# Kernel optimization log

Measured on AMD Instinct MI355X. Metric: run time of the kernel, lower is better.

## Reference

```python
import jax, jax.numpy as jnp
import numpy as np

EPS = 1e-08

def setup_inputs() -> dict:
    key = jax.random.key(0)
    ks = jax.random.split(key, 5)
    B, T, D, L = 8, 4096, 1024, 24
    data = jax.random.normal(ks[0], (B, T, D), dtype=jnp.float32)
    W_enc = jax.random.normal(ks[1], (L, D), dtype=jnp.float32) * (1.0 / np.sqrt(D))
    b_enc = jax.random.normal(ks[2], (L,), dtype=jnp.float32) * 0.01
    W_dec = jax.random.normal(ks[3], (D, L), dtype=jnp.float32) * (1.0 / np.sqrt(L))
    b_dec = jax.random.normal(ks[4], (D,), dtype=jnp.float32) * 0.01
    ecs = jnp.array([0.1], dtype=jnp.float32)  # error_correction_strength
    ep = jnp.array([1.0], dtype=jnp.float32)   # energy_preservation
    return {"data": data, "W_enc": W_enc, "b_enc": b_enc,
            "W_dec": W_dec, "b_dec": b_dec,
            "error_correction_strength": ecs, "energy_preservation": ep}

def _l2(x):
    return jnp.linalg.norm(x, axis=-1, keepdims=True)

def reference(data, W_enc, b_enc, W_dec, b_dec, error_correction_strength, energy_preservation):
    ecs = error_correction_strength[0]
    ep = energy_preservation[0]
    # --- encode_to_lattice ---
    in_e = _l2(data)                                   # [B,T,1]
    proj = jnp.einsum('btd,ld->btl', data, W_enc) + b_enc
    lattice_points = jnp.round(proj / ecs) * ecs       # quantize to lattice grid
    out_e = _l2(lattice_points)
    lattice = lattice_points * (in_e / (out_e + EPS)) * ep
    # --- decode_from_lattice ---
    in_e2 = _l2(lattice)
    corrected = jnp.where(jnp.abs(lattice) > ecs, lattice, 0.0)
    res = jnp.einsum('btl,dl->btd', corrected, W_dec) + b_dec
    out_e2 = _l2(res)
    return res * (in_e2 / (out_e2 + EPS)) * ep
```

## Files before the change

### kernel.cpp

```cpp
#include <hip/hip_runtime.h>
#include <math.h>

#define EPS 1e-8f


__global__ void prep_transpose(const float* __restrict__ W_enc, float* __restrict__ wt) {
    int i = blockIdx.x * 256 + threadIdx.x;
    if (i < 24576) {
        int k = i / 24, l = i - k * 24;
        wt[i] = W_enc[l * 1024 + k];
    }
}

__global__ void prep_gram(const float* __restrict__ Wd, const float* __restrict__ bd,
                          float* __restrict__ G, float* __restrict__ h, float* __restrict__ bb) {
    int b = blockIdx.x;
    int lane = threadIdx.x;
    float s = 0.f;
    if (b < 576) {
        int l = b / 24, m = b - (b / 24) * 24;
        for (int d = lane; d < 1024; d += 64) s = fmaf(Wd[d * 24 + l], Wd[d * 24 + m], s);
    } else if (b < 600) {
        int l = b - 576;
        for (int d = lane; d < 1024; d += 64) s = fmaf(Wd[d * 24 + l], bd[d], s);
    } else {
        for (int d = lane; d < 1024; d += 64) s = fmaf(bd[d], bd[d], s);
    }
    for (int off = 32; off; off >>= 1) s += __shfl_down(s, off);
    if (lane == 0) {
        if (b < 576) G[b] = s;
        else if (b < 600) h[b - 576] = s;
        else *bb = s;
    }
}


constexpr int LD_TILE   = 33;
constexpr int TILE_F    = 64 * LD_TILE;
constexpr int COMB_BASE = 4 * TILE_F;
constexpr int COMB_LD   = 65;
constexpr int SMEM_F    = COMB_BASE + 4 * 25 * COMB_LD;

__global__ __launch_bounds__(256, 2)
void leech_main(const float* __restrict__ data,
                const float* __restrict__ b_enc,
                const float* __restrict__ Wd,
                const float* __restrict__ b_dec,
                const float* __restrict__ ecs_p,
                const float* __restrict__ ep_p,
                const float* __restrict__ wt,
                const float* __restrict__ G,
                const float* __restrict__ h,
                const float* __restrict__ bbp,
                float* __restrict__ out)
{
    __shared__ float smem[SMEM_F];
    const int tid = threadIdx.x;
    const int w = tid >> 6;
    const int r = tid & 63;
    const int rowbase = blockIdx.x * 64;

    float* tile = smem + w * TILE_F;

    float proj[24];
#pragma unroll
    for (int l = 0; l < 24; ++l) proj[l] = 0.f;
    float ssq = 0.f;

    const int lrow = r >> 3;
    const int lk   = (r & 7) * 4;

    for (int sc = 0; sc < 8; ++sc) {
        const int k0 = w * 256 + sc * 32;
#pragma unroll
        for (int it = 0; it < 8; ++it) {
            const int row = it * 8 + lrow;
            const float4 v = *reinterpret_cast<const float4*>(
                data + (size_t)(rowbase + row) * 1024 + k0 + lk);
            float* t = tile + row * LD_TILE + lk;
            t[0] = v.x; t[1] = v.y; t[2] = v.z; t[3] = v.w;
        }
        __syncthreads();
        const float* xrow = tile + r * LD_TILE;
        const int kofs = __builtin_amdgcn_readfirstlane(k0);
#pragma unroll 4
        for (int kk = 0; kk < 32; ++kk) {
            const float x = xrow[kk];
            ssq = fmaf(x, x, ssq);
            const float* wp = wt + (size_t)(kofs + kk) * 24;
#pragma unroll
            for (int l = 0; l < 24; ++l)
                proj[l] = fmaf(wp[l], x, proj[l]);
        }
        __syncthreads();
    }

#pragma unroll
    for (int l = 0; l < 24; ++l)
        smem[COMB_BASE + (w * 25 + l) * COMB_LD + r] = proj[l];
    smem[COMB_BASE + (w * 25 + 24) * COMB_LD + r] = ssq;
    __syncthreads();

    float p[24];
#pragma unroll
    for (int l = 0; l < 24; ++l)
        p[l] = (smem[COMB_BASE + (0 * 25 + l) * COMB_LD + r] +
                smem[COMB_BASE + (1 * 25 + l) * COMB_LD + r]) +
               (smem[COMB_BASE + (2 * 25 + l) * COMB_LD + r] +
                smem[COMB_BASE + (3 * 25 + l) * COMB_LD + r]);
    const float ss = (smem[COMB_BASE + (0 * 25 + 24) * COMB_LD + r] +
                      smem[COMB_BASE + (1 * 25 + 24) * COMB_LD + r]) +
                     (smem[COMB_BASE + (2 * 25 + 24) * COMB_LD + r] +
                      smem[COMB_BASE + (3 * 25 + 24) * COMB_LD + r]);

    const float ecs = ecs_p[0];
    const float ep  = ep_p[0];
    const float in_e = sqrtf(ss);

    float lp[24]; float oe = 0.f;
#pragma unroll
    for (int l = 0; l < 24; ++l) {
        const float pp = p[l] + b_enc[l];
        const float q = rintf(pp / ecs) * ecs;
        lp[l] = q;
        oe = fmaf(q, q, oe);
    }
    const float s1 = in_e / (sqrtf(oe) + EPS) * ep;

    float c[24]; float ie = 0.f;
#pragma unroll
    for (int l = 0; l < 24; ++l) {
        const float lat = lp[l] * s1;
        ie = fmaf(lat, lat, ie);
        c[l] = (fabsf(lat) > ecs) ? lat : 0.f;
    }
    const float in_e2 = sqrtf(ie);

    float qacc = bbp[0];
#pragma unroll
    for (int l = 0; l < 24; ++l) {
        float s = 2.f * h[l];
#pragma unroll
        for (int m = 0; m < 24; ++m)
            s = fmaf(G[l * 24 + m], c[m], s);
        qacc = fmaf(s, c[l], qacc);
    }
    const float out_e2 = sqrtf(fmaxf(qacc, 0.f));
    const float s2 = in_e2 / (out_e2 + EPS) * ep;

    for (int sc = 0; sc < 8; ++sc) {
        const int d0 = __builtin_amdgcn_readfirstlane(w * 256 + sc * 32);
        __syncthreads();
        float* trow = tile + r * LD_TILE;
#pragma unroll 4
        for (int dd = 0; dd < 32; ++dd) {
            const int d = d0 + dd;
            const float* wr = Wd + d * 24;
            float acc = b_dec[d];
#pragma unroll
            for (int l = 0; l < 24; ++l)
                acc = fmaf(wr[l], c[l], acc);
            trow[dd] = acc * s2;
        }
        __syncthreads();
#pragma unroll
        for (int it = 0; it < 8; ++it) {
            const int row = it * 8 + lrow;
            const float* t = tile + row * LD_TILE + lk;
            float4 v; v.x = t[0]; v.y = t[1]; v.z = t[2]; v.w = t[3];
            *reinterpret_cast<float4*>(out + (size_t)(rowbase + row) * 1024 + d0 + lk) = v;
        }
    }
}


extern "C" void kernel_launch(void* const* d_in, const int* in_sizes, int n_in,
                              void* d_out, int out_size, void* d_ws, size_t ws_size,
                              hipStream_t stream) {
    const float* data  = (const float*)d_in[0];
    const float* W_enc = (const float*)d_in[1];
    const float* b_enc = (const float*)d_in[2];
    const float* W_dec = (const float*)d_in[3];
    const float* b_dec = (const float*)d_in[4];
    const float* ecs   = (const float*)d_in[5];
    const float* ep    = (const float*)d_in[6];
    float* out = (float*)d_out;

    float* ws = (float*)d_ws;
    float* wt = ws;
    float* G  = ws + 24576;
    float* h  = ws + 25152;
    float* bb = ws + 25176;

    const int rows = in_sizes[0] / 1024;

    hipLaunchKernelGGL(prep_transpose, dim3(96), dim3(256), 0, stream, W_enc, wt);
    hipLaunchKernelGGL(prep_gram, dim3(601), dim3(64), 0, stream, W_dec, b_dec, G, h, bb);
    hipLaunchKernelGGL(leech_main, dim3(rows / 64), dim3(256), 0, stream,
                       data, b_enc, W_dec, b_dec, ecs, ep, wt, G, h, bb, out);
}
```

Baseline: 343.9 us.

## Prefetch input tiles into registers, drop block barriers, raise occupancy, merge prep kernels

The main kernel now double-buffers each wave's next 32-column input slice in registers while it computes on the current slice held in LDS. It also removes the block-wide __syncthreads in the encode and decode loops, since each wave only touches its own tile. The cross-wave reduction reuses the tile area instead of a separate LDS region, and the launch bound rises from 2 to 4 blocks per CU. The two prep kernels are merged into one launch. The barrier removal relies on lanes within a wave seeing each other's LDS writes in order without an explicit barrier. The extra register buffers may also cap occupancy below the requested level.

```diff
diff --git a/kernel.cpp b/kernel.cpp
--- a/kernel.cpp
+++ b/kernel.cpp
@@ -3,19 +3,19 @@
 
 #define EPS 1e-8f
 
-
-__global__ void prep_transpose(const float* __restrict__ W_enc, float* __restrict__ wt) {
-    int i = blockIdx.x * 256 + threadIdx.x;
-    if (i < 24576) {
+__global__ void prep_all(const float* __restrict__ W_enc,
+                         const float* __restrict__ Wd, const float* __restrict__ bd,
+                         float* __restrict__ wt, float* __restrict__ G,
+                         float* __restrict__ h, float* __restrict__ bb) {
+    int b = blockIdx.x;
+    int lane = threadIdx.x;
+    if (b < 384) {
+        int i = b * 64 + lane;
         int k = i / 24, l = i - k * 24;
         wt[i] = W_enc[l * 1024 + k];
-    }
-}
-
-__global__ void prep_gram(const float* __restrict__ Wd, const float* __restrict__ bd,
-                          float* __restrict__ G, float* __restrict__ h, float* __restrict__ bb) {
-    int b = blockIdx.x;
-    int lane = threadIdx.x;
+        return;
+    }
+    b -= 384;
     float s = 0.f;
     if (b < 576) {
         int l = b / 24, m = b - (b / 24) * 24;
@@ -35,13 +35,11 @@
 }
 
 
-constexpr int LD_TILE   = 33;
-constexpr int TILE_F    = 64 * LD_TILE;
-constexpr int COMB_BASE = 4 * TILE_F;
-constexpr int COMB_LD   = 65;
-constexpr int SMEM_F    = COMB_BASE + 4 * 25 * COMB_LD;
-
-__global__ __launch_bounds__(256, 2)
+constexpr int LD_TILE = 33;
+constexpr int TILE_F  = 64 * LD_TILE;
+constexpr int SMEM_F  = 4 * TILE_F;
+
+__global__ __launch_bounds__(256, 4)
 void leech_main(const float* __restrict__ data,
                 const float* __restrict__ b_enc,
                 const float* __restrict__ Wd,
@@ -62,28 +60,38 @@
 
     float* tile = smem + w * TILE_F;
 
+    const int lrow = r >> 3;
+    const int lk   = (r & 7) * 4;
+
     float proj[24];
 #pragma unroll
     for (int l = 0; l < 24; ++l) proj[l] = 0.f;
     float ssq = 0.f;
 
-    const int lrow = r >> 3;
-    const int lk   = (r & 7) * 4;
+    const int kw = __builtin_amdgcn_readfirstlane((tid >> 6) * 256);
+
+    float4 buf[8];
+#pragma unroll
+    for (int it = 0; it < 8; ++it)
+        buf[it] = *reinterpret_cast<const float4*>(
+            data + (size_t)(rowbase + it * 8 + lrow) * 1024 + kw + lk);
 
     for (int sc = 0; sc < 8; ++sc) {
-        const int k0 = w * 256 + sc * 32;
 #pragma unroll
         for (int it = 0; it < 8; ++it) {
-            const int row = it * 8 + lrow;
-            const float4 v = *reinterpret_cast<const float4*>(
-                data + (size_t)(rowbase + row) * 1024 + k0 + lk);
-            float* t = tile + row * LD_TILE + lk;
-            t[0] = v.x; t[1] = v.y; t[2] = v.z; t[3] = v.w;
-        }
-        __syncthreads();
+            float* t = tile + (it * 8 + lrow) * LD_TILE + lk;
+            t[0] = buf[it].x; t[1] = buf[it].y; t[2] = buf[it].z; t[3] = buf[it].w;
+        }
+        if (sc < 7) {
+            const int k0n = kw + (sc + 1) * 32;
+#pragma unroll
+            for (int it = 0; it < 8; ++it)
+                buf[it] = *reinterpret_cast<const float4*>(
+                    data + (size_t)(rowbase + it * 8 + lrow) * 1024 + k0n + lk);
+        }
         const float* xrow = tile + r * LD_TILE;
-        const int kofs = __builtin_amdgcn_readfirstlane(k0);
-#pragma unroll 4
+        const int kofs = __builtin_amdgcn_readfirstlane(kw + sc * 32);
+#pragma unroll 8
         for (int kk = 0; kk < 32; ++kk) {
             const float x = xrow[kk];
             ssq = fmaf(x, x, ssq);
@@ -92,26 +100,22 @@
             for (int l = 0; l < 24; ++l)
                 proj[l] = fmaf(wp[l], x, proj[l]);
         }
-        __syncthreads();
     }
 
 #pragma unroll
     for (int l = 0; l < 24; ++l)
-        smem[COMB_BASE + (w * 25 + l) * COMB_LD + r] = proj[l];
-    smem[COMB_BASE + (w * 25 + 24) * COMB_LD + r] = ssq;
+        smem[w * TILE_F + l * 64 + r] = proj[l];
+    smem[w * TILE_F + 24 * 64 + r] = ssq;
     __syncthreads();
 
     float p[24];
 #pragma unroll
     for (int l = 0; l < 24; ++l)
-        p[l] = (smem[COMB_BASE + (0 * 25 + l) * COMB_LD + r] +
-                smem[COMB_BASE + (1 * 25 + l) * COMB_LD + r]) +
-               (smem[COMB_BASE + (2 * 25 + l) * COMB_LD + r] +
-                smem[COMB_BASE + (3 * 25 + l) * COMB_LD + r]);
-    const float ss = (smem[COMB_BASE + (0 * 25 + 24) * COMB_LD + r] +
-                      smem[COMB_BASE + (1 * 25 + 24) * COMB_LD + r]) +
-                     (smem[COMB_BASE + (2 * 25 + 24) * COMB_LD + r] +
-                      smem[COMB_BASE + (3 * 25 + 24) * COMB_LD + r]);
+        p[l] = (smem[0 * TILE_F + l * 64 + r] + smem[1 * TILE_F + l * 64 + r]) +
+               (smem[2 * TILE_F + l * 64 + r] + smem[3 * TILE_F + l * 64 + r]);
+    const float ss = (smem[0 * TILE_F + 24 * 64 + r] + smem[1 * TILE_F + 24 * 64 + r]) +
+                     (smem[2 * TILE_F + 24 * 64 + r] + smem[3 * TILE_F + 24 * 64 + r]);
+    __syncthreads();
 
     const float ecs = ecs_p[0];
     const float ep  = ep_p[0];
@@ -149,8 +153,7 @@
     const float s2 = in_e2 / (out_e2 + EPS) * ep;
 
     for (int sc = 0; sc < 8; ++sc) {
-        const int d0 = __builtin_amdgcn_readfirstlane(w * 256 + sc * 32);
-        __syncthreads();
+        const int d0 = __builtin_amdgcn_readfirstlane(kw + sc * 32);
         float* trow = tile + r * LD_TILE;
 #pragma unroll 4
         for (int dd = 0; dd < 32; ++dd) {
@@ -162,13 +165,12 @@
                 acc = fmaf(wr[l], c[l], acc);
             trow[dd] = acc * s2;
         }
-        __syncthreads();
 #pragma unroll
         for (int it = 0; it < 8; ++it) {
-            const int row = it * 8 + lrow;
-            const float* t = tile + row * LD_TILE + lk;
+            const float* t = tile + (it * 8 + lrow) * LD_TILE + lk;
             float4 v; v.x = t[0]; v.y = t[1]; v.z = t[2]; v.w = t[3];
-            *reinterpret_cast<float4*>(out + (size_t)(rowbase + row) * 1024 + d0 + lk) = v;
+            *reinterpret_cast<float4*>(
+                out + (size_t)(rowbase + it * 8 + lrow) * 1024 + d0 + lk) = v;
         }
     }
 }
@@ -194,8 +196,8 @@
 
     const int rows = in_sizes[0] / 1024;
 
-    hipLaunchKernelGGL(prep_transpose, dim3(96), dim3(256), 0, stream, W_enc, wt);
-    hipLaunchKernelGGL(prep_gram, dim3(601), dim3(64), 0, stream, W_dec, b_dec, G, h, bb);
+    hipLaunchKernelGGL(prep_all, dim3(985), dim3(64), 0, stream,
+                       W_enc, W_dec, b_dec, wt, G, h, bb);
     hipLaunchKernelGGL(leech_main, dim3(rows / 64), dim3(256), 0, stream,
                        data, b_enc, W_dec, b_dec, ecs, ep, wt, G, h, bb, out);
 }
```

New measurement: 323.7 us. -5.9%, faster.
